# Optimization experiments

Measured on AMD Instinct MI355X. Metric: run time of the kernel, lower is better.

## Reference

```python
import jax, jax.numpy as jnp
import numpy as np

N, L, P = 1024, 4096, 8192  # batch, simulated length, acquired spectrum length


def batch_linspace(a, b, n):
    # a, b: [..., 1] -> [..., n]
    t = jnp.arange(n, dtype=jnp.float32) / (n - 1)
    return a + (b - a) * t


def bounded_random_walk(start, end, std, lower, upper, noise):
    """Vectorized bounded random walk with reflecting bounds.
    start/end/std/lower/upper: [N]; noise: [N, L] uniform(0,1) steps."""
    n = noise.shape[-1]
    rand = jnp.cumsum(std[:, None] * (noise - 0.5), axis=-1)          # [N, L]
    rand_trend = batch_linspace(rand[:, :1], rand[:, -1:], n)
    deltas = rand - rand_trend                                         # detrended walk
    bounds = (upper - lower)[:, None]
    span = deltas.max(-1, keepdims=True) - deltas.min(-1, keepdims=True)
    deltas = deltas / jnp.maximum(1.0, span / bounds)                  # squeeze into bound width
    trend = batch_linspace(start[:, None], end[:, None], n)
    ub = upper[:, None] - trend
    lb = lower[:, None] - trend
    over = deltas - ub
    deltas = jnp.where(over >= 0, ub - over, deltas)                   # reflect off upper bound
    under = lb - deltas
    deltas = jnp.where(under >= 0, lb + under, deltas)                 # reflect off lower bound
    return trend + deltas


def batch_smooth(x, w):
    """Per-sample box-filter smoothing with zero ('constant') padding.
    x: [N, L] float; w: [N] int window sizes."""
    n, l = x.shape
    xp = jnp.pad(x, ((0, 0), (l, l)))
    cs = jnp.concatenate([jnp.zeros((n, 1), x.dtype), jnp.cumsum(xp, -1)], -1)
    t = jnp.arange(l)
    lo = t[None, :] - w[:, None] // 2 + l                              # [N, L]
    hi = lo + w[:, None]
    box = jnp.take_along_axis(cs, hi, 1) - jnp.take_along_axis(cs, lo, 1)
    return box / w[:, None].astype(x.dtype)


def normalize_max(x):
    denom = jnp.max(jnp.abs(x), axis=-1, keepdims=True)
    return x / jnp.where(denom == 0, 1.0, denom)


def sim2acquired(sig, ppm_lo, ppm_hi, ppm):
    """Map simulated signal on [ppm_lo, ppm_hi] grid onto full acquired ppm axis
    (linear interp, zero outside simulated range)."""
    l = sig.shape[-1]
    xs = jnp.linspace(ppm_lo, ppm_hi, l)
    return jax.vmap(lambda s: jnp.interp(ppm, xs, s, left=0.0, right=0.0))(sig)


def hilbert(x):
    """FFT-based analytic signal; returns stacked [N, 2, P] (real, imag)."""
    p = x.shape[-1]
    h = jnp.zeros(p, x.dtype).at[0].set(1.0).at[p // 2].set(1.0).at[1:p // 2].set(2.0)
    a = jnp.fft.ifft(jnp.fft.fft(x, axis=-1) * h, axis=-1)
    return jnp.stack([jnp.real(a), jnp.imag(a)], axis=1)


def setup_inputs() -> dict:
    key = jax.random.key(0)
    ks = jax.random.split(key, 10)
    u = lambda k, lo, hi: jax.random.uniform(k, (N,), minval=lo, maxval=hi, dtype=jnp.float32)
    start = u(ks[0], -1.0, 1.0)
    end = u(ks[1], -1.0, 1.0)
    std = u(ks[2], 0.05, 0.3)
    lower_bnd = u(ks[3], -2.0, -1.5)
    upper_bnd = u(ks[4], 1.5, 2.0)
    windows = jax.random.randint(ks[5], (N,), 8, 128, dtype=jnp.int32)
    scale = u(ks[6], 0.5, 2.0)
    noise = jax.random.uniform(ks[7], (N, L), dtype=jnp.float32)
    omit_mask = (jax.random.uniform(ks[8], (N,)) > 0.1).astype(jnp.float32)  # drop_prob=0.1
    ppm = jnp.linspace(-2.0, 10.0, P).astype(jnp.float32)                     # acquired ppm axis
    ppm_range = jnp.array([0.2, 4.2], jnp.float32)                            # simulated range
    return dict(start=start, end=end, std=std, lower_bnd=lower_bnd,
                upper_bnd=upper_bnd, windows=windows, scale=scale, noise=noise,
                omit_mask=omit_mask, ppm=ppm, ppm_range=ppm_range)


def reference(start, end, std, lower_bnd, upper_bnd, windows, scale, noise,
              omit_mask, ppm, ppm_range):
    walk = bounded_random_walk(start, end, std, lower_bnd, upper_bnd, noise)  # [N, L]
    b = batch_smooth(walk, windows)
    trend = batch_linspace(b[:, :1], b[:, -1:], b.shape[-1])
    b = normalize_max(b - trend)
    b = b * omit_mask[:, None]                                                # rand_omit
    acq = sim2acquired(b * scale[:, None], ppm_range[0], ppm_range[1], ppm)   # [N, P]
    raw = hilbert(acq)                                                        # [N, 2, P]
    return (jnp.flip(raw, axis=-1), raw)
```

## Files before the change

### kernel.cpp

```cpp
#include <hip/hip_runtime.h>

#define NB 1024
#define LL 4096
#define PP 8192
#define FN 4096

#define PIF 3.14159265358979323846f

__device__ __forceinline__ float2 cadd(float2 a, float2 b){ return make_float2(a.x+b.x, a.y+b.y); }
__device__ __forceinline__ float2 csub(float2 a, float2 b){ return make_float2(a.x-b.x, a.y-b.y); }
__device__ __forceinline__ float2 cmul(float2 a, float2 b){ return make_float2(a.x*b.x - a.y*b.y, a.x*b.y + a.y*b.x); }

__device__ __forceinline__ int PH2(int p){ return p + 2*(p >> 4); }

__device__ __forceinline__ int rev8(int k){
    return ((k & 7) << 9) | (((k >> 3) & 7) << 6) | (((k >> 6) & 7) << 3) | ((k >> 9) & 7);
}

__device__ __forceinline__ void core8f(float2* x){
    const float c8 = 0.70710678118654752f;
    float2 e0=cadd(x[0],x[4]), e1=cadd(x[1],x[5]), e2=cadd(x[2],x[6]), e3=cadd(x[3],x[7]);
    float2 o0=csub(x[0],x[4]), o1=csub(x[1],x[5]), o2=csub(x[2],x[6]), o3=csub(x[3],x[7]);
    float2 t1 = make_float2(c8*(o1.x + o1.y), c8*(o1.y - o1.x));
    float2 t2 = make_float2(o2.y, -o2.x);
    float2 t3 = make_float2(c8*(o3.y - o3.x), -c8*(o3.x + o3.y));
    float2 a0=cadd(e0,e2), a1=cadd(e1,e3), a2=csub(e0,e2), a3=csub(e1,e3);
    x[0]=cadd(a0,a1); x[4]=csub(a0,a1);
    x[2]=make_float2(a2.x + a3.y, a2.y - a3.x);
    x[6]=make_float2(a2.x - a3.y, a2.y + a3.x);
    float2 b0=cadd(o0,t2), b1=cadd(t1,t3), b2=csub(o0,t2), b3=csub(t1,t3);
    x[1]=cadd(b0,b1); x[5]=csub(b0,b1);
    x[3]=make_float2(b2.x + b3.y, b2.y - b3.x);
    x[7]=make_float2(b2.x - b3.y, b2.y + b3.x);
}
__device__ __forceinline__ void core8i(float2* x){
    const float c8 = 0.70710678118654752f;
    float2 e0=cadd(x[0],x[4]), e1=cadd(x[1],x[5]), e2=cadd(x[2],x[6]), e3=cadd(x[3],x[7]);
    float2 o0=csub(x[0],x[4]), o1=csub(x[1],x[5]), o2=csub(x[2],x[6]), o3=csub(x[3],x[7]);
    float2 t1 = make_float2(c8*(o1.x - o1.y), c8*(o1.y + o1.x));
    float2 t2 = make_float2(-o2.y, o2.x);
    float2 t3 = make_float2(-c8*(o3.x + o3.y), c8*(o3.x - o3.y));
    float2 a0=cadd(e0,e2), a1=cadd(e1,e3), a2=csub(e0,e2), a3=csub(e1,e3);
    x[0]=cadd(a0,a1); x[4]=csub(a0,a1);
    x[2]=make_float2(a2.x - a3.y, a2.y + a3.x);
    x[6]=make_float2(a2.x + a3.y, a2.y - a3.x);
    float2 b0=cadd(o0,t2), b1=cadd(t1,t3), b2=csub(o0,t2), b3=csub(t1,t3);
    x[1]=cadd(b0,b1); x[5]=csub(b0,b1);
    x[3]=make_float2(b2.x - b3.y, b2.y + b3.x);
    x[7]=make_float2(b2.x + b3.y, b2.y - b3.x);
}

__global__ __launch_bounds__(512, 8) void k_all(
    const float* __restrict__ g_start,
    const float* __restrict__ g_end,
    const float* __restrict__ g_std,
    const float* __restrict__ g_low,
    const float* __restrict__ g_up,
    const int*   __restrict__ g_win,
    const float* __restrict__ g_scale,
    const float* __restrict__ g_noise,
    const float* __restrict__ g_omit,
    const float* __restrict__ g_ppm,
    const float* __restrict__ g_ppmr,
    float* __restrict__ g_out)
{
    __shared__ alignas(16) float2 buf[4608];
    float* bf  = (float*)buf;
#define CSI(t) ((t) + ((t) >> 5))
    float* cs  = bf;
    float* tmp = bf + 4226;
    float* shv = bf + 4242;

    const int n    = blockIdx.x;
    const int tid  = threadIdx.x;
    const int lane = tid & 63;
    const int wid  = tid >> 6;
    const float st = g_start[n];
    const float en = g_end[n];
    const float sd = g_std[n];
    const float lo = g_low[n];
    const float up = g_up[n];
    const int   w  = g_win[n];
    const float inv_nm1 = 1.0f / (float)(LL - 1);

    float r[8];
    {
        const float4* p = (const float4*)(g_noise + (size_t)n * LL) + (size_t)tid * 2;
        float4 ta = p[0], tb = p[1];
        r[0]=ta.x; r[1]=ta.y; r[2]=ta.z; r[3]=ta.w;
        r[4]=tb.x; r[5]=tb.y; r[6]=tb.z; r[7]=tb.w;
    }
#pragma unroll
    for (int k = 0; k < 8; k++) r[k] = sd * (r[k] - 0.5f);

    float run = 0.0f;
#pragma unroll
    for (int k = 0; k < 8; k++) { run += r[k]; r[k] = run; }
    float ws = run;
#pragma unroll
    for (int off = 1; off < 64; off <<= 1) { float t = __shfl_up(ws, off); if (lane >= off) ws += t; }
    if (lane == 63) tmp[wid] = ws;
    if (tid == 0)   shv[0] = r[0];
    __syncthreads();
    float t0=tmp[0],t1=tmp[1],t2=tmp[2],t3=tmp[3],t4=tmp[4],t5=tmp[5],t6=tmp[6],t7=tmp[7];
    const float rT = ((t0+t1)+(t2+t3))+((t4+t5)+(t6+t7));
    const float r0 = shv[0];
    float base = (wid>0?t0:0.f)+(wid>1?t1:0.f)+(wid>2?t2:0.f)+(wid>3?t3:0.f)
               + (wid>4?t4:0.f)+(wid>5?t5:0.f)+(wid>6?t6:0.f);
    float excl = base + ws - run;
    __syncthreads();

    float mx = -INFINITY, mn = INFINITY;
#pragma unroll
    for (int k = 0; k < 8; k++) {
        int t = tid * 8 + k;
        float d = (excl + r[k]) - (r0 + (rT - r0) * ((float)t * inv_nm1));
        r[k] = d;
        mx = fmaxf(mx, d); mn = fminf(mn, d);
    }
#pragma unroll
    for (int off = 32; off > 0; off >>= 1) {
        mx = fmaxf(mx, __shfl_xor(mx, off));
        mn = fminf(mn, __shfl_xor(mn, off));
    }
    if (lane == 0) { tmp[wid] = mx; tmp[8 + wid] = mn; }
    __syncthreads();
    mx = fmaxf(fmaxf(fmaxf(tmp[0],tmp[1]),fmaxf(tmp[2],tmp[3])),
               fmaxf(fmaxf(tmp[4],tmp[5]),fmaxf(tmp[6],tmp[7])));
    mn = fminf(fminf(fminf(tmp[8],tmp[9]),fminf(tmp[10],tmp[11])),
               fminf(fminf(tmp[12],tmp[13]),fminf(tmp[14],tmp[15])));
    __syncthreads();

    const float qs = fmaxf(1.0f, (mx - mn) / (up - lo));

#pragma unroll
    for (int k = 0; k < 8; k++) {
        int t = tid * 8 + k;
        float tr  = st + (en - st) * ((float)t * inv_nm1);
        float ub  = up - tr;
        float lb2 = lo - tr;
        float d = r[k] / qs;
        float over = d - ub;
        d = (over >= 0.0f) ? (ub - over) : d;
        float under = lb2 - d;
        d = (under >= 0.0f) ? (lb2 + under) : d;
        r[k] = tr + d;
    }

    run = 0.0f;
#pragma unroll
    for (int k = 0; k < 8; k++) { run += r[k]; r[k] = run; }
    ws = run;
#pragma unroll
    for (int off = 1; off < 64; off <<= 1) { float t = __shfl_up(ws, off); if (lane >= off) ws += t; }
    if (lane == 63) tmp[wid] = ws;
    __syncthreads();
    t0=tmp[0];t1=tmp[1];t2=tmp[2];t3=tmp[3];t4=tmp[4];t5=tmp[5];t6=tmp[6];t7=tmp[7];
    const float grand2 = ((t0+t1)+(t2+t3))+((t4+t5)+(t6+t7));
    base = (wid>0?t0:0.f)+(wid>1?t1:0.f)+(wid>2?t2:0.f)+(wid>3?t3:0.f)
         + (wid>4?t4:0.f)+(wid>5?t5:0.f)+(wid>6?t6:0.f);
    float excl2 = base + ws - run;
#pragma unroll
    for (int k = 0; k < 8; k++) {
        int t = tid * 8 + k;
        cs[CSI(t)] = excl2 + ((k == 0) ? 0.0f : r[k - 1]);
    }
    if (tid == 511) cs[CSI(LL)] = grand2;
    __syncthreads();

    const int wh = w / 2;
    const float invw = 1.0f / (float)w;
#pragma unroll
    for (int k = 0; k < 8; k++) {
        int t  = tid + 512 * k;
        int li = t - wh;
        int hi = li + w;
        li = (li < 0) ? 0 : li;
        hi = (hi > LL) ? LL : hi;
        r[k] = (cs[CSI(hi)] - cs[CSI(li)]) * invw;
    }
    if (tid == 0)   shv[0] = r[0];
    if (tid == 511) shv[1] = r[7];
    __syncthreads();
    const float b0 = shv[0], bL = shv[1];

    float am = 0.0f;
#pragma unroll
    for (int k = 0; k < 8; k++) {
        int t = tid + 512 * k;
        r[k] -= b0 + (bL - b0) * ((float)t * inv_nm1);
        am = fmaxf(am, fabsf(r[k]));
    }
#pragma unroll
    for (int off = 32; off > 0; off >>= 1) am = fmaxf(am, __shfl_xor(am, off));
    if (lane == 0) tmp[wid] = am;
    __syncthreads();
    float denom = fmaxf(fmaxf(fmaxf(tmp[0],tmp[1]),fmaxf(tmp[2],tmp[3])),
                        fmaxf(fmaxf(tmp[4],tmp[5]),fmaxf(tmp[6],tmp[7])));
    denom = (denom == 0.0f) ? 1.0f : denom;
    const float fac = g_omit[n] * g_scale[n] / denom;
    __syncthreads();

#pragma unroll
    for (int k = 0; k < 8; k++) {
        int t = tid + 512 * k;
        bf[t] = r[k] * fac;
    }
    __syncthreads();

    const float xlo = g_ppmr[0];
    const float xhi = g_ppmr[1];
    const float posmul = (float)(LL - 1) / (xhi - xlo);
    const size_t base1 = (size_t)NB * 2 * PP + (size_t)n * 2 * PP;
    const size_t base0 = (size_t)n * 2 * PP;

    auto interp1 = [&](float x) -> float {
        if (x < xlo || x > xhi) return 0.0f;
        float pos = (x - xlo) * posmul;
        int idx = (int)floorf(pos);
        idx = (idx < 0) ? 0 : ((idx > LL - 2) ? (LL - 2) : idx);
        float fr = pos - (float)idx;
        float s0 = bf[idx], s1 = bf[idx + 1];
        return s0 + (s1 - s0) * fr;
    };

    float2 X[8];
#pragma unroll
    for (int m = 0; m < 8; m++) {
        int p = tid + 512 * m;
        float2 pm = *(const float2*)(g_ppm + 2 * p);
        float re0 = interp1(pm.x);
        float re1 = interp1(pm.y);
        X[m] = make_float2(re0, re1);
        *(float2*)(g_out + base1 + 2 * p)          = make_float2(re0, re1);
        *(float2*)(g_out + base0 + PP - 2 - 2 * p) = make_float2(re1, re0);
    }
    __syncthreads();

    const int bA = tid + 2 * (tid >> 4);
    {
        core8f(X);
        float sn, cn; __sincosf((-PIF / 2048.0f) * (float)tid, &sn, &cn);
        float2 E = make_float2(cn, sn), Er = E;
        buf[bA]        = X[0];
        buf[bA +  576] = cmul(X[1], Er); Er = cmul(Er, E);
        buf[bA + 1152] = cmul(X[2], Er); Er = cmul(Er, E);
        buf[bA + 1728] = cmul(X[3], Er); Er = cmul(Er, E);
        buf[bA + 2304] = cmul(X[4], Er); Er = cmul(Er, E);
        buf[bA + 2880] = cmul(X[5], Er); Er = cmul(Er, E);
        buf[bA + 3456] = cmul(X[6], Er); Er = cmul(Er, E);
        buf[bA + 4032] = cmul(X[7], Er);
    }
    __syncthreads();

    const int j2 = tid & 63;
    const int bB = (tid >> 6) * 576 + j2 + 2 * (j2 >> 4);
    {
#pragma unroll
        for (int d = 0; d < 8; d++) X[d] = buf[bB + 72 * d];
        core8f(X);
        float sn, cn; __sincosf((-PIF / 256.0f) * (float)j2, &sn, &cn);
        float2 E = make_float2(cn, sn), Er = E;
        buf[bB]       = X[0];
        buf[bB +  72] = cmul(X[1], Er); Er = cmul(Er, E);
        buf[bB + 144] = cmul(X[2], Er); Er = cmul(Er, E);
        buf[bB + 216] = cmul(X[3], Er); Er = cmul(Er, E);
        buf[bB + 288] = cmul(X[4], Er); Er = cmul(Er, E);
        buf[bB + 360] = cmul(X[5], Er); Er = cmul(Er, E);
        buf[bB + 432] = cmul(X[6], Er); Er = cmul(Er, E);
        buf[bB + 504] = cmul(X[7], Er);
    }
    __syncthreads();

    const int j3 = tid & 7;
    const int bC = (tid >> 3) * 72 + j3;
    {
        X[0]=buf[bC];    X[1]=buf[bC+8];  X[2]=buf[bC+18]; X[3]=buf[bC+26];
        X[4]=buf[bC+36]; X[5]=buf[bC+44]; X[6]=buf[bC+54]; X[7]=buf[bC+62];
        core8f(X);
        float sn, cn; __sincosf((-PIF / 32.0f) * (float)j3, &sn, &cn);
        float2 E = make_float2(cn, sn), Er = E;
        buf[bC]    = X[0];
        buf[bC+ 8] = cmul(X[1], Er); Er = cmul(Er, E);
        buf[bC+18] = cmul(X[2], Er); Er = cmul(Er, E);
        buf[bC+26] = cmul(X[3], Er); Er = cmul(Er, E);
        buf[bC+36] = cmul(X[4], Er); Er = cmul(Er, E);
        buf[bC+44] = cmul(X[5], Er); Er = cmul(Er, E);
        buf[bC+54] = cmul(X[6], Er); Er = cmul(Er, E);
        buf[bC+62] = cmul(X[7], Er);
    }
    __syncthreads();

    const int f4 = 4 * tid + (tid >> 1);
    float4* b4 = reinterpret_cast<float4*>(buf);
    {
        float4 a0 = b4[f4], a1 = b4[f4+1], a2 = b4[f4+2], a3 = b4[f4+3];
        X[0]=make_float2(a0.x,a0.y); X[1]=make_float2(a0.z,a0.w);
        X[2]=make_float2(a1.x,a1.y); X[3]=make_float2(a1.z,a1.w);
        X[4]=make_float2(a2.x,a2.y); X[5]=make_float2(a2.z,a2.w);
        X[6]=make_float2(a3.x,a3.y); X[7]=make_float2(a3.z,a3.w);
        core8f(X);
        b4[f4]   = make_float4(X[0].x,X[0].y,X[1].x,X[1].y);
        b4[f4+1] = make_float4(X[2].x,X[2].y,X[3].x,X[3].y);
        b4[f4+2] = make_float4(X[4].x,X[4].y,X[5].x,X[5].y);
        b4[f4+3] = make_float4(X[6].x,X[6].y,X[7].x,X[7].y);
    }
    __syncthreads();

    {
        const float s = 1.0f / (2.0f * (float)FN);
#pragma unroll
        for (int m = 0; m < 4; m++) {
            int k = ((tid & 31) << 6) | ((tid >> 5) << 2) | m;
            if (k == 0) {
                buf[0] = make_float2(0.0f, 0.0f);
                float2 Z = buf[4];
                buf[4] = make_float2(-2.0f*s*Z.y, 2.0f*s*Z.x);
            } else {
                int pk = PH2(rev8(k));
                int pj = PH2(rev8(FN - k));
                float2 Zk = buf[pk];
                float2 Zj = buf[pj];
                float ux = Zk.x + Zj.x, uy = Zk.y - Zj.y;
                float vx = Zk.x - Zj.x, vy = Zk.y + Zj.y;
                float sn, cn; __sincosf((PIF/(float)FN) * (float)k, &sn, &cn);
                float2 zk, zj;
                zk.x = s * ((ux*cn - uy*sn) - (vx*cn + vy*sn));
                zk.y = s * ((ux*sn + uy*cn) + (vx*sn - vy*cn));
                float u2x = ux,  u2y = -uy;
                float v2x = -vx, v2y = vy;
                zj.x = s * ((v2x*cn - v2y*sn) - (u2x*cn + u2y*sn));
                zj.y = s * ((v2x*sn + v2y*cn) + (u2x*sn - u2y*cn));
                buf[pk] = zk;
                buf[pj] = zj;
            }
        }
    }
    __syncthreads();

    {
        float4 a0 = b4[f4], a1 = b4[f4+1], a2 = b4[f4+2], a3 = b4[f4+3];
        X[0]=make_float2(a0.x,a0.y); X[1]=make_float2(a0.z,a0.w);
        X[2]=make_float2(a1.x,a1.y); X[3]=make_float2(a1.z,a1.w);
        X[4]=make_float2(a2.x,a2.y); X[5]=make_float2(a2.z,a2.w);
        X[6]=make_float2(a3.x,a3.y); X[7]=make_float2(a3.z,a3.w);
        core8i(X);
        b4[f4]   = make_float4(X[0].x,X[0].y,X[1].x,X[1].y);
        b4[f4+1] = make_float4(X[2].x,X[2].y,X[3].x,X[3].y);
        b4[f4+2] = make_float4(X[4].x,X[4].y,X[5].x,X[5].y);
        b4[f4+3] = make_float4(X[6].x,X[6].y,X[7].x,X[7].y);
    }
    __syncthreads();

    {
        X[0]=buf[bC];    X[1]=buf[bC+8];  X[2]=buf[bC+18]; X[3]=buf[bC+26];
        X[4]=buf[bC+36]; X[5]=buf[bC+44]; X[6]=buf[bC+54]; X[7]=buf[bC+62];
        float sn, cn; __sincosf((PIF / 32.0f) * (float)j3, &sn, &cn);
        float2 E = make_float2(cn, sn), Er = E;
        X[1]=cmul(X[1],Er); Er=cmul(Er,E);
        X[2]=cmul(X[2],Er); Er=cmul(Er,E);
        X[3]=cmul(X[3],Er); Er=cmul(Er,E);
        X[4]=cmul(X[4],Er); Er=cmul(Er,E);
        X[5]=cmul(X[5],Er); Er=cmul(Er,E);
        X[6]=cmul(X[6],Er); Er=cmul(Er,E);
        X[7]=cmul(X[7],Er);
        core8i(X);
        buf[bC]=X[0];    buf[bC+8]=X[1];  buf[bC+18]=X[2]; buf[bC+26]=X[3];
        buf[bC+36]=X[4]; buf[bC+44]=X[5]; buf[bC+54]=X[6]; buf[bC+62]=X[7];
    }
    __syncthreads();

    {
#pragma unroll
        for (int d = 0; d < 8; d++) X[d] = buf[bB + 72 * d];
        float sn, cn; __sincosf((PIF / 256.0f) * (float)j2, &sn, &cn);
        float2 E = make_float2(cn, sn), Er = E;
        X[1]=cmul(X[1],Er); Er=cmul(Er,E);
        X[2]=cmul(X[2],Er); Er=cmul(Er,E);
        X[3]=cmul(X[3],Er); Er=cmul(Er,E);
        X[4]=cmul(X[4],Er); Er=cmul(Er,E);
        X[5]=cmul(X[5],Er); Er=cmul(Er,E);
        X[6]=cmul(X[6],Er); Er=cmul(Er,E);
        X[7]=cmul(X[7],Er);
        core8i(X);
#pragma unroll
        for (int d = 0; d < 8; d++) buf[bB + 72 * d] = X[d];
    }
    __syncthreads();

    {
#pragma unroll
        for (int d = 0; d < 8; d++) X[d] = buf[bA + 576 * d];
        float sn, cn; __sincosf((PIF / 2048.0f) * (float)tid, &sn, &cn);
        float2 E = make_float2(cn, sn), Er = E;
        X[1]=cmul(X[1],Er); Er=cmul(Er,E);
        X[2]=cmul(X[2],Er); Er=cmul(Er,E);
        X[3]=cmul(X[3],Er); Er=cmul(Er,E);
        X[4]=cmul(X[4],Er); Er=cmul(Er,E);
        X[5]=cmul(X[5],Er); Er=cmul(Er,E);
        X[6]=cmul(X[6],Er); Er=cmul(Er,E);
        X[7]=cmul(X[7],Er);
        core8i(X);
#pragma unroll
        for (int d = 0; d < 8; d++) {
            int p = tid + 512 * d;
            float2 vv = X[d];
            *(float2*)(g_out + base1 + PP + 2 * p)         = vv;
            *(float2*)(g_out + base0 + 2 * PP - 2 - 2 * p) = make_float2(vv.y, vv.x);
        }
    }
}

extern "C" void kernel_launch(void* const* d_in, const int* in_sizes, int n_in,
                              void* d_out, int out_size, void* d_ws, size_t ws_size,
                              hipStream_t stream)
{
    const float* start = (const float*)d_in[0];
    const float* end_  = (const float*)d_in[1];
    const float* stdv  = (const float*)d_in[2];
    const float* lowb  = (const float*)d_in[3];
    const float* upb   = (const float*)d_in[4];
    const int*   win   = (const int*)d_in[5];
    const float* scl   = (const float*)d_in[6];
    const float* noise = (const float*)d_in[7];
    const float* omit  = (const float*)d_in[8];
    const float* ppm   = (const float*)d_in[9];
    const float* ppmr  = (const float*)d_in[10];
    float* out = (float*)d_out;

    hipLaunchKernelGGL(k_all, dim3(NB), dim3(512), 0, stream,
                       start, end_, stdv, lowb, upb, win, scl, noise, omit,
                       ppm, ppmr, out);
}
```

Baseline: 175.8 us.

## Remove redundant block barriers and use wave-local fences in FFT stages

Gives each block-wide reduction its own scratch slots so the trailing __syncthreads after each reduction can go, and recomputes the smoothed endpoint values directly from the prefix-sum array so a broadcast barrier is no longer needed. Several FFT-stage __syncthreads calls are replaced with a wave-only barrier plus a compiler memory fence, on the assumption that those stages only exchange data within a single 64-lane wave. This cuts block-wide synchronisation cost. If any of those FFT stages actually reads shared-memory data written by another wave, results will be wrong.

New measurement: 174.3 us. Within noise of the previous version (-0.9%).

```diff
diff --git a/kernel.cpp b/kernel.cpp
--- a/kernel.cpp
+++ b/kernel.cpp
@@ -10,6 +10,8 @@
 __device__ __forceinline__ float2 cadd(float2 a, float2 b){ return make_float2(a.x+b.x, a.y+b.y); }
 __device__ __forceinline__ float2 csub(float2 a, float2 b){ return make_float2(a.x-b.x, a.y-b.y); }
 __device__ __forceinline__ float2 cmul(float2 a, float2 b){ return make_float2(a.x*b.x - a.y*b.y, a.x*b.y + a.y*b.x); }
+
+#define WFENCE() do { __builtin_amdgcn_wave_barrier(); asm volatile("" ::: "memory"); } while (0)
 
 __device__ __forceinline__ int PH2(int p){ return p + 2*(p >> 4); }
 
@@ -67,9 +69,12 @@
     __shared__ alignas(16) float2 buf[4608];
     float* bf  = (float*)buf;
 #define CSI(t) ((t) + ((t) >> 5))
-    float* cs  = bf;
-    float* tmp = bf + 4226;
-    float* shv = bf + 4242;
+    float* cs   = bf;
+    float* tmp1 = bf + 4226;
+    float* tmp2 = bf + 4240;
+    float* tmp3 = bf + 4256;
+    float* tmp4 = bf + 4264;
+    float* shv  = bf + 4272;
 
     const int n    = blockIdx.x;
     const int tid  = threadIdx.x;
@@ -99,16 +104,15 @@
     float ws = run;
 #pragma unroll
     for (int off = 1; off < 64; off <<= 1) { float t = __shfl_up(ws, off); if (lane >= off) ws += t; }
-    if (lane == 63) tmp[wid] = ws;
+    if (lane == 63) tmp1[wid] = ws;
     if (tid == 0)   shv[0] = r[0];
     __syncthreads();
-    float t0=tmp[0],t1=tmp[1],t2=tmp[2],t3=tmp[3],t4=tmp[4],t5=tmp[5],t6=tmp[6],t7=tmp[7];
+    float t0=tmp1[0],t1=tmp1[1],t2=tmp1[2],t3=tmp1[3],t4=tmp1[4],t5=tmp1[5],t6=tmp1[6],t7=tmp1[7];
     const float rT = ((t0+t1)+(t2+t3))+((t4+t5)+(t6+t7));
     const float r0 = shv[0];
     float base = (wid>0?t0:0.f)+(wid>1?t1:0.f)+(wid>2?t2:0.f)+(wid>3?t3:0.f)
                + (wid>4?t4:0.f)+(wid>5?t5:0.f)+(wid>6?t6:0.f);
     float excl = base + ws - run;
-    __syncthreads();
 
     float mx = -INFINITY, mn = INFINITY;
 #pragma unroll
@@ -123,13 +127,12 @@
         mx = fmaxf(mx, __shfl_xor(mx, off));
         mn = fminf(mn, __shfl_xor(mn, off));
     }
-    if (lane == 0) { tmp[wid] = mx; tmp[8 + wid] = mn; }
-    __syncthreads();
-    mx = fmaxf(fmaxf(fmaxf(tmp[0],tmp[1]),fmaxf(tmp[2],tmp[3])),
-               fmaxf(fmaxf(tmp[4],tmp[5]),fmaxf(tmp[6],tmp[7])));
-    mn = fminf(fminf(fminf(tmp[8],tmp[9]),fminf(tmp[10],tmp[11])),
-               fminf(fminf(tmp[12],tmp[13]),fminf(tmp[14],tmp[15])));
-    __syncthreads();
+    if (lane == 0) { tmp2[wid] = mx; tmp2[8 + wid] = mn; }
+    __syncthreads();
+    mx = fmaxf(fmaxf(fmaxf(tmp2[0],tmp2[1]),fmaxf(tmp2[2],tmp2[3])),
+               fmaxf(fmaxf(tmp2[4],tmp2[5]),fmaxf(tmp2[6],tmp2[7])));
+    mn = fminf(fminf(fminf(tmp2[8],tmp2[9]),fminf(tmp2[10],tmp2[11])),
+               fminf(fminf(tmp2[12],tmp2[13]),fminf(tmp2[14],tmp2[15])));
 
     const float qs = fmaxf(1.0f, (mx - mn) / (up - lo));
 
@@ -153,9 +156,9 @@
     ws = run;
 #pragma unroll
     for (int off = 1; off < 64; off <<= 1) { float t = __shfl_up(ws, off); if (lane >= off) ws += t; }
-    if (lane == 63) tmp[wid] = ws;
-    __syncthreads();
-    t0=tmp[0];t1=tmp[1];t2=tmp[2];t3=tmp[3];t4=tmp[4];t5=tmp[5];t6=tmp[6];t7=tmp[7];
+    if (lane == 63) tmp3[wid] = ws;
+    __syncthreads();
+    t0=tmp3[0];t1=tmp3[1];t2=tmp3[2];t3=tmp3[3];t4=tmp3[4];t5=tmp3[5];t6=tmp3[6];t7=tmp3[7];
     const float grand2 = ((t0+t1)+(t2+t3))+((t4+t5)+(t6+t7));
     base = (wid>0?t0:0.f)+(wid>1?t1:0.f)+(wid>2?t2:0.f)+(wid>3?t3:0.f)
          + (wid>4?t4:0.f)+(wid>5?t5:0.f)+(wid>6?t6:0.f);
@@ -179,27 +182,30 @@
         hi = (hi > LL) ? LL : hi;
         r[k] = (cs[CSI(hi)] - cs[CSI(li)]) * invw;
     }
-    if (tid == 0)   shv[0] = r[0];
-    if (tid == 511) shv[1] = r[7];
-    __syncthreads();
-    const float b0 = shv[0], bL = shv[1];
+    float b0v, bLv;
+    {
+        int hi0 = w - wh;
+        b0v = (cs[CSI(hi0)] - cs[CSI(0)]) * invw;
+        int liL = LL - 1 - wh;
+        int hiL = liL + w; if (hiL > LL) hiL = LL;
+        bLv = (cs[CSI(hiL)] - cs[CSI(liL)]) * invw;
+    }
 
     float am = 0.0f;
 #pragma unroll
     for (int k = 0; k < 8; k++) {
         int t = tid + 512 * k;
-        r[k] -= b0 + (bL - b0) * ((float)t * inv_nm1);
+        r[k] -= b0v + (bLv - b0v) * ((float)t * inv_nm1);
         am = fmaxf(am, fabsf(r[k]));
     }
 #pragma unroll
     for (int off = 32; off > 0; off >>= 1) am = fmaxf(am, __shfl_xor(am, off));
-    if (lane == 0) tmp[wid] = am;
-    __syncthreads();
-    float denom = fmaxf(fmaxf(fmaxf(tmp[0],tmp[1]),fmaxf(tmp[2],tmp[3])),
-                        fmaxf(fmaxf(tmp[4],tmp[5]),fmaxf(tmp[6],tmp[7])));
+    if (lane == 0) tmp4[wid] = am;
+    __syncthreads();
+    float denom = fmaxf(fmaxf(fmaxf(tmp4[0],tmp4[1]),fmaxf(tmp4[2],tmp4[3])),
+                        fmaxf(fmaxf(tmp4[4],tmp4[5]),fmaxf(tmp4[6],tmp4[7])));
     denom = (denom == 0.0f) ? 1.0f : denom;
     const float fac = g_omit[n] * g_scale[n] / denom;
-    __syncthreads();
 
 #pragma unroll
     for (int k = 0; k < 8; k++) {
@@ -270,7 +276,7 @@
         buf[bB + 432] = cmul(X[6], Er); Er = cmul(Er, E);
         buf[bB + 504] = cmul(X[7], Er);
     }
-    __syncthreads();
+    WFENCE();
 
     const int j3 = tid & 7;
     const int bC = (tid >> 3) * 72 + j3;
@@ -289,7 +295,7 @@
         buf[bC+54] = cmul(X[6], Er); Er = cmul(Er, E);
         buf[bC+62] = cmul(X[7], Er);
     }
-    __syncthreads();
+    WFENCE();
 
     const int f4 = 4 * tid + (tid >> 1);
     float4* b4 = reinterpret_cast<float4*>(buf);
@@ -350,7 +356,7 @@
         b4[f4+2] = make_float4(X[4].x,X[4].y,X[5].x,X[5].y);
         b4[f4+3] = make_float4(X[6].x,X[6].y,X[7].x,X[7].y);
     }
-    __syncthreads();
+    WFENCE();
 
     {
         X[0]=buf[bC];    X[1]=buf[bC+8];  X[2]=buf[bC+18]; X[3]=buf[bC+26];
@@ -368,7 +374,7 @@
         buf[bC]=X[0];    buf[bC+8]=X[1];  buf[bC+18]=X[2]; buf[bC+26]=X[3];
         buf[bC+36]=X[4]; buf[bC+44]=X[5]; buf[bC+54]=X[6]; buf[bC+62]=X[7];
     }
-    __syncthreads();
+    WFENCE();
 
     {
 #pragma unroll
```
